# Kernel optimization log

Measured on AMD Instinct MI355X. Metric: run time of the kernel, lower is better.

## Reference

```python
import jax, jax.numpy as jnp
import numpy as np

B, H, W, C = 2, 128, 128, 96
L = H * W
NUM_HEADS = 6
D_STATE = 16
DT_RANK = 6  # ceil(96/16)
D_CONV = 4
MLP_HIDDEN = 4 * C


def _layernorm(x, g, b, eps=1e-5):
    m = x.mean(-1, keepdims=True)
    v = x.var(-1, keepdims=True)
    return (x - m) * jax.lax.rsqrt(v + eps) * g + b


def _dwconv2d(x, w, b):
    # x: [B,C,H,W], w: [C,1,3,3] depthwise, padding=1 (torch 'same' for k=3)
    y = jax.lax.conv_general_dilated(x, w, (1, 1), [(1, 1), (1, 1)],
                                     dimension_numbers=('NCHW', 'OIHW', 'NCHW'),
                                     feature_group_count=x.shape[1])
    return y + b[None, :, None, None]


def _dwconv1d(x, w):
    # x: [B,C,L], w: [C,1,4]; torch padding='same' for even k=4 pads (1,2); bias is None (conv_bias//2 == 0)
    return jax.lax.conv_general_dilated(x, w, (1,), [(1, 2)],
                                        dimension_numbers=('NCH', 'OIH', 'NCH'),
                                        feature_group_count=x.shape[1])


def _rope(x):
    # x: [b, H, W, c]; 2D axial rotary embedding, k_max = c//4 per axis
    b, h, w, c = x.shape
    k_max = c // 4
    theta = 1.0 / (10000.0 ** (jnp.arange(k_max, dtype=jnp.float32) / k_max))
    ang_h = jnp.broadcast_to(jnp.arange(h, dtype=jnp.float32)[:, None, None] * theta, (h, w, k_max))
    ang_w = jnp.broadcast_to(jnp.arange(w, dtype=jnp.float32)[None, :, None] * theta, (h, w, k_max))
    angles = jnp.concatenate([ang_h, ang_w], -1)  # [h,w,c//2]
    cos, sin = jnp.cos(angles), jnp.sin(angles)
    xr, xi = x[..., 0::2], x[..., 1::2]  # consecutive pairs -> complex
    out_r = xr * cos - xi * sin
    out_i = xr * sin + xi * cos
    return jnp.stack([out_r, out_i], -1).reshape(x.shape)


def _linear_attention(x, qk_w, qk_b, lepe_w, lepe_b):
    # x: [b, n, c]
    b, n, c = x.shape
    hd = c // NUM_HEADS
    qk = x @ qk_w + qk_b  # [b,n,2c]
    q = jax.nn.elu(qk[..., :c]) + 1.0
    k = jax.nn.elu(qk[..., c:]) + 1.0
    v = x
    q_r = _rope(q.reshape(b, H, W, c)).reshape(b, n, NUM_HEADS, hd).transpose(0, 2, 1, 3)
    k_r = _rope(k.reshape(b, H, W, c)).reshape(b, n, NUM_HEADS, hd).transpose(0, 2, 1, 3)
    qh = q.reshape(b, n, NUM_HEADS, hd).transpose(0, 2, 1, 3)
    kh = k.reshape(b, n, NUM_HEADS, hd).transpose(0, 2, 1, 3)
    vh = v.reshape(b, n, NUM_HEADS, hd).transpose(0, 2, 1, 3)
    kmean = kh.mean(axis=2, keepdims=True)  # [b,h,1,hd]
    zden = 1.0 / (jnp.einsum('bhnd,bhmd->bhnm', qh, kmean) + 1e-6)  # [b,h,n,1]
    scale = n ** (-0.5)
    kv = jnp.einsum('bhnd,bhne->bhde', k_r * scale, vh * scale)  # [b,h,hd,hd]
    out = jnp.einsum('bhnd,bhde->bhne', q_r, kv) * zden
    out = out.transpose(0, 2, 1, 3).reshape(b, n, c)
    v2d = v.reshape(b, H, W, c).transpose(0, 3, 1, 2)
    lepe = _dwconv2d(v2d, lepe_w, lepe_b).transpose(0, 2, 3, 1).reshape(b, n, c)
    return out + lepe


def _selective_scan(u, delta, A, Bm, Cm, Dv):
    # u, delta: [b,d,l]; A: [d,n]; Bm, Cm: [b,n,l]; Dv: [d]
    dA = jnp.exp(jnp.einsum('bdl,dn->lbdn', delta, A))
    dBu = jnp.einsum('bdl,bnl,bdl->lbdn', delta, Bm, u)
    Ct = jnp.moveaxis(Cm, -1, 0)  # [l,b,n]

    def step(hcar, inp):
        dA_t, dBu_t, C_t = inp
        hcar = dA_t * hcar + dBu_t  # [b,d,n]
        y_t = jnp.einsum('bdn,bn->bd', hcar, C_t)
        return hcar, y_t

    h0 = jnp.zeros(dA.shape[1:], dtype=u.dtype)
    _, ys = jax.lax.scan(step, h0, (dA, dBu, Ct))  # ys: [l,b,d]
    y = jnp.moveaxis(ys, 0, -1)  # [b,d,l]
    return y + Dv[None, :, None] * u


def setup_inputs() -> dict:
    key = jax.random.key(0)
    ks = iter(jax.random.split(key, 40))

    def rn(shape, s=0.02):
        return jax.random.normal(next(ks), shape, jnp.float32) * s

    dt = jnp.exp(jax.random.uniform(next(ks), (C,), jnp.float32)
                 * (np.log(0.1) - np.log(0.001)) + np.log(0.001))
    dt_proj_b = dt + jnp.log(-jnp.expm1(-dt))
    return {
        'hidden_states': jax.random.normal(next(ks), (B, L, C), jnp.float32),
        'norm_in_g': jnp.ones((C,), jnp.float32),
        'norm_in_b': jnp.zeros((C,), jnp.float32),
        'in_proj_w': rn((C, 3 * C)),
        'dw_w': rn((C, 1, 3, 3)),
        'dw_b': rn((C,)),
        'qk_w': rn((C, 2 * C)),
        'qk_b': rn((2 * C,)),
        'lepe_w': rn((C, 1, 3, 3)),
        'lepe_b': rn((C,)),
        'conv_x_w': rn((C, 1, D_CONV)),
        'conv_z_w': rn((C, 1, D_CONV)),
        'x_proj_w': rn((C, DT_RANK + 2 * D_STATE)),
        'dt_proj_w': rn((DT_RANK, C), DT_RANK ** -0.5),
        'dt_proj_b': dt_proj_b,
        'A_log': jnp.log(jnp.broadcast_to(jnp.arange(1, D_STATE + 1, dtype=jnp.float32), (C, D_STATE)) + 0.0),
        'D': jnp.ones((C,), jnp.float32),
        'out_proj_w': rn((2 * C, C)),
        'proj_out_w': rn((C, C)),
        'proj_out_b': rn((C,)),
        'out_w': rn((2 * C, C)),
        'out_b': rn((C,)),
        'norm_mlp_g': jnp.ones((C,), jnp.float32),
        'norm_mlp_b': jnp.zeros((C,), jnp.float32),
        'fc1_w': rn((C, MLP_HIDDEN)),
        'fc1_b': rn((MLP_HIDDEN,)),
        'fc2_w': rn((MLP_HIDDEN, C)),
        'fc2_b': rn((C,)),
    }


def reference(hidden_states, norm_in_g, norm_in_b, in_proj_w, dw_w, dw_b, qk_w, qk_b,
              lepe_w, lepe_b, conv_x_w, conv_z_w, x_proj_w, dt_proj_w, dt_proj_b,
              A_log, D, out_proj_w, proj_out_w, proj_out_b, out_w, out_b,
              norm_mlp_g, norm_mlp_b, fc1_w, fc1_b, fc2_w, fc2_b):
    b, l, c = hidden_states.shape
    shortcut = hidden_states
    hs = _layernorm(hidden_states, norm_in_g, norm_in_b)
    xzw = jnp.transpose(hs @ in_proj_w, (0, 2, 1))  # [b,3c,l]
    x, z, w_ = jnp.split(xzw, 3, axis=1)  # each [b,c,l]
    # linear-attention branch
    lin_x = jax.nn.silu(_dwconv2d(w_.reshape(b, c, H, W), dw_w, dw_b))
    lin_x = jnp.transpose(lin_x, (0, 2, 3, 1)).reshape(b, l, c)
    lin_x = _linear_attention(lin_x, qk_w, qk_b, lepe_w, lepe_b)
    # selective-scan branch
    A = -jnp.exp(A_log)
    x = jax.nn.silu(_dwconv1d(x, conv_x_w))
    z = jax.nn.silu(_dwconv1d(z, conv_z_w))
    x_dbl = jnp.einsum('bdl,de->ble', x, x_proj_w)
    dt = x_dbl[..., :DT_RANK]
    Bm = jnp.transpose(x_dbl[..., DT_RANK:DT_RANK + D_STATE], (0, 2, 1))
    Cm = jnp.transpose(x_dbl[..., DT_RANK + D_STATE:], (0, 2, 1))
    delta = jax.nn.softplus(jnp.einsum('blr,rd->bdl', dt, dt_proj_w) + dt_proj_b[None, :, None])
    y = _selective_scan(x, delta, A, Bm, Cm, D)
    y = jnp.concatenate([y, z], axis=1)  # [b,2c,l]
    out1 = jnp.transpose(y, (0, 2, 1)) @ out_proj_w  # [b,l,c]
    z_t = jnp.transpose(z, (0, 2, 1))
    out2 = (lin_x * z_t) @ proj_out_w + proj_out_b
    out = jnp.concatenate([out1, out2], -1) @ out_w + out_b
    out = shortcut + out
    h2 = _layernorm(out, norm_mlp_g, norm_mlp_b)
    h2 = jax.nn.gelu(h2 @ fc1_w + fc1_b, approximate=False)
    return out + (h2 @ fc2_w + fc2_b)
```

## Files before the change

kernel.cpp:

```cpp
#include <hip/hip_runtime.h>
#include <hip/hip_bf16.h>
#include <hip/hip_fp16.h>
#include <math.h>

#define B_ 2
#define H_ 128
#define W_ 128
#define C_ 96
#define L_ (H_*W_)
#define BL_ (B_*L_)
#define NH_ 6
#define NPROJ_ 38
#define MLPH_ 384
#define NCH_ 512
#define CHL_ (L_/NCH_)
#define NG_ 32

typedef __attribute__((ext_vector_type(8))) short bf16x8;
typedef __attribute__((ext_vector_type(4))) float f32x4;
typedef __attribute__((ext_vector_type(4))) unsigned short us4v;

#define MFMA16(a,b,c) __builtin_amdgcn_mfma_f32_16x16x32_bf16(a,b,c,0,0,0)

#define WOFF1 0
#define WOFF2 54
#define WOFF3 90
#define WOFF4 126
#define WOFF5 144
#define WOFF6 180
#define WOFF7 252
#define WOFF8 324
#define WFRAGS 333

__device__ __forceinline__ float siluf(float x){ return x / (1.f + __expf(-x)); }
__device__ __forceinline__ unsigned short f2bf(float x){
    __hip_bfloat16 h = __float2bfloat16(x);
    return *reinterpret_cast<unsigned short*>(&h);
}
__device__ __forceinline__ unsigned pack2(float a, float b){
    return (unsigned)f2bf(a) | ((unsigned)f2bf(b) << 16);
}
__device__ __forceinline__ float bf2f(unsigned short u){
    return __uint_as_float((unsigned)u << 16);
}
__device__ __forceinline__ unsigned short f2h(float x){
    __half h = __float2half(x);
    return *reinterpret_cast<unsigned short*>(&h);
}
__device__ __forceinline__ float h2f(unsigned short u){
    __half h = *reinterpret_cast<__half*>(&u);
    return __half2float(h);
}
__device__ __forceinline__ float gelu_fast(float x){
    float u_ = 0.7978845608f*x*(1.f + 0.044715f*x*x);
    float au = fabsf(u_);
    float e = __expf(-2.f*au);
    float th = (1.f - e)/(1.f + e);
    th = copysignf(th, u_);
    return 0.5f*x*(1.f + th);
}

__global__ __launch_bounds__(64) void k_setup(const float* __restrict__ w1,
    const float* __restrict__ w2, const float* __restrict__ w3,
    const float* __restrict__ w4, const float* __restrict__ w5,
    const float* __restrict__ w6, const float* __restrict__ w7,
    const float* __restrict__ dww, const float* __restrict__ lw,
    const float* __restrict__ xpw, const float* __restrict__ cxw,
    const float* __restrict__ czw,
    unsigned short* __restrict__ dst, float2* __restrict__ ctab,
    float* __restrict__ wt9, float* __restrict__ lw9, float* __restrict__ kvacc,
    float* __restrict__ wxT, float* __restrict__ wzT)
{
    int m = blockIdx.y;
    int l = threadIdx.x;
    if (m < 7){
        const float* srcs[7] = {w1,w2,w3,w4,w5,w6,w7};
        const int Ks[7]   = {96,96,192,96,192,96,384};
        const int Ns[7]   = {288,192,96,96,96,384,96};
        const int offs[7] = {WOFF1,WOFF2,WOFF3,WOFF4,WOFF5,WOFF6,WOFF7};
        int f = blockIdx.x;
        int nnt = Ns[m] >> 4, nkf = Ks[m] >> 5;
        if (f >= nnt*nkf) return;
        int kf = f / nnt, nt = f - kf*nnt;
        const float* s = srcs[m];
        unsigned short* d = dst + ((size_t)(offs[m] + f)*64 + l)*8;
        int krow = kf*32 + (l>>4)*8;
        int col  = nt*16 + (l&15);
        #pragma unroll
        for (int j=0;j<8;j++) d[j] = f2bf(s[(size_t)(krow+j)*Ns[m] + col]);
    } else {
        int x = blockIdx.x;
        if (x == 0){
            for (int i=l; i<128*24; i+=64){
                int pos = i/24, p = i%24;
                float th = powf(10000.f, -(float)p/24.f);
                float sn, cs; sincosf((float)pos*th, &sn, &cs);
                ctab[i] = make_float2(cs, sn);
            }
        } else if (x == 1){
            for (int i=l; i<3264; i+=64) kvacc[i] = 0.f;
        } else if (x == 2){
            for (int i=l; i<864; i+=64){
                int c = i/9, tap = i%9;
                wt9[tap*96 + c] = dww[i];
                lw9[tap*96 + c] = lw[i];
            }
        } else if (x == 3){
            for (int f=0; f<9; f++){
                int kf=f/3, nt=f%3;
                unsigned short* d = dst + ((size_t)(WOFF8 + f)*64 + l)*8;
                int krow = kf*32 + (l>>4)*8;
                int col  = nt*16 + (l&15);
                #pragma unroll
                for (int j=0;j<8;j++){
                    float v = (col < NPROJ_) ? xpw[(size_t)(krow+j)*NPROJ_ + col] : 0.f;
                    d[j] = f2bf(v);
                }
            }
        } else if (x == 4){
            for (int i=l; i<384; i+=64){
                int j = i/96, c = i%96;
                wxT[i] = cxw[c*4 + j];
                wzT[i] = czw[c*4 + j];
            }
        }
    }
}

__global__ __launch_bounds__(256) void k_ln_inproj_m(const float* __restrict__ hs,
    const float* __restrict__ gg, const float* __restrict__ bb,
    const unsigned short* __restrict__ wbf,
    unsigned short* __restrict__ xx, unsigned short* __restrict__ zz,
    unsigned short* __restrict__ ww)
{
    __shared__ unsigned short A[64*128];
    int t = threadIdx.x;
    size_t row0 = (size_t)blockIdx.x * 64;
    {
        int r = t >> 2, q = t & 3;
        const float* src = hs + (row0 + r)*C_ + q*24;
        float v[24];
        float s=0.f, s2=0.f;
        #pragma unroll
        for (int i=0;i<24;i++){ float x=src[i]; v[i]=x; s+=x; s2+=x*x; }
        s += __shfl_xor(s,1); s2 += __shfl_xor(s2,1);
        s += __shfl_xor(s,2); s2 += __shfl_xor(s2,2);
        float mn = s*(1.f/C_);
        float rs = rsqrtf(s2*(1.f/C_) - mn*mn + 1e-5f);
        int base = r*128, sw = (r&7)<<3;
        #pragma unroll
        for (int i=0;i<24;i+=2){
            int c = q*24 + i;
            float a0 = (v[i]  -mn)*rs*gg[c]   + bb[c];
            float a1 = (v[i+1]-mn)*rs*gg[c+1] + bb[c+1];
            *(unsigned*)&A[base + (c ^ sw)] = pack2(a0,a1);
        }
    }
    __syncthreads();
    int w = t>>6, l = t&63, lr = l&15, lh = l>>4;
    int arow = w*16 + lr;
    int abase = arow*128, asw = (arow&7)<<3;
    bf16x8 af[3];
    #pragma unroll
    for (int kf=0;kf<3;kf++)
        af[kf] = *(const bf16x8*)&A[abase + ((kf*32 + lh*8) ^ asw)];
    #pragma unroll 2
    for (int nt=0; nt<18; nt++){
        f32x4 acc = {0.f,0.f,0.f,0.f};
        #pragma unroll
        for (int kf=0;kf<3;kf++){
            bf16x8 bf_ = *(const bf16x8*)(wbf + ((size_t)((WOFF1 + kf*18 + nt)*64 + l))*8);
            acc = MFMA16(af[kf], bf_, acc);
        }
        unsigned short* base_;
        if (nt < 6) base_ = xx; else if (nt < 12) base_ = zz; else base_ = ww;
        int col = (nt%6)*16 + lr;
        unsigned short* dst = base_ + (row0 + w*16 + lh*4)*C_ + col;
        #pragma unroll
        for (int j=0;j<4;j++) dst[(size_t)j*C_] = f2bf(acc[j]);
    }
}

__global__ __launch_bounds__(256) void k_dwconv2d(const unsigned short* __restrict__ wwb,
    const float* __restrict__ wt9, const float* __restrict__ dwb,
    unsigned short* __restrict__ out)
{
    int gid = blockIdx.x*256 + threadIdx.x;
    int row = gid/24, c4 = gid%24; int c = c4*4;
    int b = row >> 14;
    int ll = row & (L_-1);
    int h = ll >> 7, wq = ll & 127;
    float a0=0.f,a1=0.f,a2=0.f,a3=0.f;
    #pragma unroll
    for (int kh=0; kh<3; kh++){
        int hh = h + kh - 1;
        if ((unsigned)hh < 128u){
            int base_row = (b<<14) + (hh<<7);
            #pragma unroll
            for (int kw=0; kw<3; kw++){
                int wp = wq + kw - 1;
                if ((unsigned)wp < 128u){
                    us4v v = *(const us4v*)&wwb[(size_t)(base_row + wp)*C_ + c];
                    float4 wt = *(const float4*)&wt9[(kh*3+kw)*96 + c];
                    a0 += bf2f(v[0])*wt.x; a1 += bf2f(v[1])*wt.y;
                    a2 += bf2f(v[2])*wt.z; a3 += bf2f(v[3])*wt.w;
                }
            }
        }
    }
    float4 bv = *(const float4*)&dwb[c];
    us4v o;
    o[0]=f2bf(siluf(a0+bv.x)); o[1]=f2bf(siluf(a1+bv.y));
    o[2]=f2bf(siluf(a2+bv.z)); o[3]=f2bf(siluf(a3+bv.w));
    *(us4v*)&out[(size_t)row*C_ + c] = o;
}

__global__ __launch_bounds__(384) void k_conv1d_xdbl(const unsigned short* __restrict__ xxb,
    const unsigned short* __restrict__ zzb, const float* __restrict__ wxT,
    const float* __restrict__ wzT, const unsigned short* __restrict__ wbf,
    const float* __restrict__ dtw, const float* __restrict__ dtb,
    const float* __restrict__ A_log,
    unsigned short* __restrict__ xsb, unsigned short* __restrict__ zb,
    unsigned short* __restrict__ dlh, float* __restrict__ BC,
    float* __restrict__ Ap, float* __restrict__ Be)
{
    __shared__ unsigned short A[64*128];
    __shared__ float XD[64][8];
    __shared__ float dtws[6][96];
    __shared__ float sdl[64][96];
    __shared__ float sbc[64][32];
    int t = threadIdx.x;
    size_t row0 = (size_t)blockIdx.x * 64;
    int b = (int)(row0 >> 14);
    int l0 = (int)(row0 & 16383);
    for (int i=t; i<576; i+=384) dtws[i/96][i%96] = dtw[i];
    for (int p=t; p<64*24; p+=384){
        int r = p/24, cq = p - r*24, c = cq*4;
        int l = l0 + r;
        float ax0=0.f,ax1=0.f,ax2=0.f,ax3=0.f;
        float az0=0.f,az1=0.f,az2=0.f,az3=0.f;
        #pragma unroll
        for (int j=0;j<4;j++){
            int lq = l - 1 + j;
            if ((unsigned)lq < (unsigned)L_){
                size_t off = ((size_t)(b<<14) + lq)*C_ + c;
                us4v xv = *(const us4v*)&xxb[off];
                us4v zv = *(const us4v*)&zzb[off];
// ... 47 lines not shown
        int r = t>>2, q = t&3;
        float xd0=XD[r][0], xd1=XD[r][1], xd2=XD[r][2];
        float xd3=XD[r][3], xd4=XD[r][4], xd5=XD[r][5];
        #pragma unroll
        for (int g=0; g<6; g++){
            int c = q*24 + g*4;
            float4 acc = *(const float4*)&dtb[c];
            float4 w0 = *(const float4*)&dtws[0][c];
            float4 w1 = *(const float4*)&dtws[1][c];
            float4 w2 = *(const float4*)&dtws[2][c];
            float4 w3 = *(const float4*)&dtws[3][c];
            float4 w4 = *(const float4*)&dtws[4][c];
            float4 w5 = *(const float4*)&dtws[5][c];
            acc.x += xd0*w0.x + xd1*w1.x + xd2*w2.x + xd3*w3.x + xd4*w4.x + xd5*w5.x;
            acc.y += xd0*w0.y + xd1*w1.y + xd2*w2.y + xd3*w3.y + xd4*w4.y + xd5*w5.y;
            acc.z += xd0*w0.z + xd1*w1.z + xd2*w2.z + xd3*w3.z + xd4*w4.z + xd5*w5.z;
            acc.w += xd0*w0.w + xd1*w1.w + xd2*w2.w + xd3*w3.w + xd4*w4.w + xd5*w5.w;
            float4 dl;
            dl.x = (acc.x>20.f)? acc.x : __logf(1.f+__expf(acc.x));
            dl.y = (acc.y>20.f)? acc.y : __logf(1.f+__expf(acc.y));
            dl.z = (acc.z>20.f)? acc.z : __logf(1.f+__expf(acc.z));
            dl.w = (acc.w>20.f)? acc.w : __logf(1.f+__expf(acc.w));
            sdl[r][c]=dl.x; sdl[r][c+1]=dl.y; sdl[r][c+2]=dl.z; sdl[r][c+3]=dl.w;
            us4v dh; dh[0]=f2h(dl.x); dh[1]=f2h(dl.y); dh[2]=f2h(dl.z); dh[3]=f2h(dl.w);
            *(us4v*)&dlh[(row0+r)*C_ + c] = dh;
        }
    }
    __syncthreads();
    {
        int c = t>>2, nq = t&3;
        float4 a4 = *(const float4*)&A_log[c*16 + nq*4];
        float a0=-__expf(a4.x), a1=-__expf(a4.y), a2=-__expf(a4.z), a3=-__expf(a4.w);
        int chbase = b*NCH_ + (l0>>5);
        int csw_c = c;
        #pragma unroll
        for (int chunk=0; chunk<2; chunk++){
            float ap0=1.f,ap1=1.f,ap2=1.f,ap3=1.f;
            float be0=0.f,be1=0.f,be2=0.f,be3=0.f;
            for (int i=0;i<CHL_;i++){
                int row = chunk*CHL_ + i;
                float dl = sdl[row][c];
                float u = bf2f(A[row*128 + (csw_c ^ ((row&7)<<3))]);
                float du = dl*u;
                float4 bc = *(const float4*)&sbc[row][nq*4];
                float e0=__expf(dl*a0), e1=__expf(dl*a1), e2=__expf(dl*a2), e3=__expf(dl*a3);
                ap0*=e0; be0=be0*e0+du*bc.x;
                ap1*=e1; be1=be1*e1+du*bc.y;
                ap2*=e2; be2=be2*e2+du*bc.z;
                ap3*=e3; be3=be3*e3+du*bc.w;
            }
            size_t o = (size_t)(chbase+chunk)*1536 + c*16 + nq*4;
            float4 apv={ap0,ap1,ap2,ap3}, bev={be0,be1,be2,be3};
            *(float4*)&Ap[o] = apv;
            *(float4*)&Be[o] = bev;
        }
    }
}

__global__ __launch_bounds__(256) void k_qk_kv(const unsigned short* __restrict__ lin,
    const unsigned short* __restrict__ wbf, const float* __restrict__ qkb,
    const float2* __restrict__ ctab, unsigned short* __restrict__ qo,
    float* __restrict__ kvacc)
{
    __shared__ unsigned short A[64*128];
    __shared__ float KR[64*105];
    __shared__ float kmsum[96];
    int t = threadIdx.x;
    size_t row0 = (size_t)blockIdx.x * 64;
    int b = (int)(row0 >> 14);
    int l0 = (int)(row0 & 16383);
    for (int p = t; p < 64*12; p += 256){
        int r = p/12, c = (p - r*12)*8;
        int sw = (r&7)<<3;
        *(uint4*)&A[r*128 + (c ^ sw)] = *(const uint4*)&lin[(row0+r)*C_ + c];
    }
    if (t < 96) kmsum[t] = 0.f;
    __syncthreads();
    int w=t>>6, l=t&63, lr=l&15, lh=l>>4;
    int arow = w*16+lr; int asw=(arow&7)<<3;
    bf16x8 af[3];
    #pragma unroll
    for (int kf=0;kf<3;kf++)
        af[kf] = *(const bf16x8*)&A[arow*128 + ((kf*32 + lh*8) ^ asw)];
    #pragma unroll 2
    for (int nt=0; nt<12; nt++){
        f32x4 acc={0.f,0.f,0.f,0.f};
        #pragma unroll
        for (int kf=0;kf<3;kf++){
            bf16x8 bfr=*(const bf16x8*)(wbf + ((size_t)((WOFF2 + kf*12 + nt)*64 + l))*8);
            acc = MFMA16(af[kf], bfr, acc);
        }
        int colg = nt*16 + lr;
        float bias = qkb[colg];
        float vv[4];
        #pragma unroll
        for (int j=0;j<4;j++){
            float v = acc[j] + bias;
            vv[j] = (v>0.f)? v+1.f : __expf(v);
        }
        if (nt < 6){
            unsigned short* dp = qo + (row0 + w*16 + lh*4)*C_ + colg;
            #pragma unroll
            for (int j=0;j<4;j++) dp[(size_t)j*C_] = f2bf(vv[j]);
        } else {
            int ck = colg - 96;
            atomicAdd(&kmsum[ck], vv[0]+vv[1]+vv[2]+vv[3]);
            float pv[4];
// ... 104 lines not shown
                    acc.z += bf2f(v[2])*wt.z; acc.w += bf2f(v[3])*wt.w;
                }
            }
        }
    }
    us4v zu = *(const us4v*)&zb[row*C_ + c];
    us4v res;
    res[0] = f2bf((o.x*zd + acc.x)*bf2f(zu[0]));
    res[1] = f2bf((o.y*zd + acc.y)*bf2f(zu[1]));
    res[2] = f2bf((o.z*zd + acc.z)*bf2f(zu[2]));
    res[3] = f2bf((o.w*zd + acc.w)*bf2f(zu[3]));
    *(us4v*)&azb[row*C_ + c] = res;
}

__global__ __launch_bounds__(384) void k_scan2a(const float* __restrict__ Ap,
    const float* __restrict__ Be, float* __restrict__ GA, float* __restrict__ GB)
{
    int t = threadIdx.x; int blk = blockIdx.x;
    int b = blk>>5, g = blk&(NG_-1);
    int idx = (t>>2)*16 + (t&3)*4;
    float4 A = {1.f,1.f,1.f,1.f}, Bv = {0.f,0.f,0.f,0.f};
    for (int j=0;j<16;j++){
        size_t o = ((size_t)(b*NCH_ + g*16 + j))*1536 + idx;
        float4 a = *(const float4*)&Ap[o];
        float4 bb = *(const float4*)&Be[o];
        Bv.x=a.x*Bv.x+bb.x; Bv.y=a.y*Bv.y+bb.y; Bv.z=a.z*Bv.z+bb.z; Bv.w=a.w*Bv.w+bb.w;
        A.x*=a.x; A.y*=a.y; A.z*=a.z; A.w*=a.w;
    }
    size_t o = (size_t)blk*1536 + idx;
    *(float4*)&GA[o] = A;
    *(float4*)&GB[o] = Bv;
}

__global__ __launch_bounds__(256) void k_scan2b(const float* __restrict__ GA,
    const float* __restrict__ GB, float* __restrict__ Gin)
{
    int t = blockIdx.x*256 + threadIdx.x;
    int b = t/1536, m = t%1536;
    float h = 0.f;
    for (int g=0; g<NG_; g++){
        size_t o = ((size_t)(b*NG_+g))*1536 + m;
        Gin[o] = h;
        h = GA[o]*h + GB[o];
    }
}

__global__ __launch_bounds__(384) void k_scan2c(const float* __restrict__ Ap,
    const float* __restrict__ Be, const float* __restrict__ Gin,
    float* __restrict__ Hin)
{
    int t = threadIdx.x; int blk = blockIdx.x;
    int b = blk>>5, g = blk&(NG_-1);
    int idx = (t>>2)*16 + (t&3)*4;
    float4 h = *(const float4*)&Gin[(size_t)blk*1536 + idx];
    for (int j=0;j<16;j++){
        size_t o = ((size_t)(b*NCH_ + g*16 + j))*1536 + idx;
        *(float4*)&Hin[o] = h;
        float4 a = *(const float4*)&Ap[o];
        float4 bb = *(const float4*)&Be[o];
        h.x=a.x*h.x+bb.x; h.y=a.y*h.y+bb.y; h.z=a.z*h.z+bb.z; h.w=a.w*h.w+bb.w;
    }
}

__global__ __launch_bounds__(384) void k_scan3(const unsigned short* __restrict__ dlh,
    const unsigned short* __restrict__ xsb, const float* __restrict__ BC,
    const float* __restrict__ A_log, const float* __restrict__ Dv,
    const float* __restrict__ Hin, unsigned short* __restrict__ y)
{
    int t = threadIdx.x; int nq = t&3, c = t>>2;
    int blk = blockIdx.x; int b = blk>>9, ch = blk&(NCH_-1);
    float4 a4 = *(const float4*)&A_log[c*16 + nq*4];
    float a0=-__expf(a4.x), a1=-__expf(a4.y), a2=-__expf(a4.z), a3=-__expf(a4.w);
    float4 h = *(const float4*)&Hin[(size_t)blk*1536 + c*16 + nq*4];
    float Dc = Dv[c];
    size_t base = ((size_t)b<<14) + ch*CHL_;
    for (int i=0;i<CHL_;i++){
        size_t row = base + i;
        float dl = h2f(dlh[row*C_+c]);
        float u  = bf2f(xsb[row*C_+c]);
        float du = dl*u;
        float4 bcB = *(const float4*)&BC[row*32 + nq*4];
        float4 bcC = *(const float4*)&BC[row*32 + 16 + nq*4];
        float e0=__expf(dl*a0), e1=__expf(dl*a1), e2=__expf(dl*a2), e3=__expf(dl*a3);
        h.x=h.x*e0+du*bcB.x; h.y=h.y*e1+du*bcB.y;
        h.z=h.z*e2+du*bcB.z; h.w=h.w*e3+du*bcB.w;
        float yv = h.x*bcC.x + h.y*bcC.y + h.z*bcC.z + h.w*bcC.w;
        yv += __shfl_xor(yv,1);
        yv += __shfl_xor(yv,2);
        if (nq == 0) y[row*C_+c] = f2bf(yv + Dc*u);
    }
}

__global__ __launch_bounds__(512) void k_combine_mlp(const unsigned short* __restrict__ yb,
    const unsigned short* __restrict__ zb, const unsigned short* __restrict__ azb,
    const unsigned short* __restrict__ wbf, const float* __restrict__ pob,
    const float* __restrict__ outb, const float* __restrict__ hs,
    const float* __restrict__ gg, const float* __restrict__ bb,
    const float* __restrict__ f1b, const float* __restrict__ f2b,
    float* __restrict__ outr)
{
    __shared__ __attribute__((aligned(16))) char POOL[65536];
    __shared__ float LNS[64][2], LNS2[64][2];
    unsigned short* C2 = (unsigned short*)POOL;
    unsigned short* AT = (unsigned short*)POOL;
    unsigned short* HID= (unsigned short*)(POOL + 16384);
    int t=threadIdx.x;
    size_t row0=(size_t)blockIdx.x*64;
    int w=t>>6, l=t&63, lr=l&15, lh=l>>4;
    int rt=w>>1, hf=w&1;
    int arow=rt*16+lr; int asw=(arow&7)<<3;
    size_t gbase = (row0+arow)*C_;
    bf16x8 af1[6], af2[3];
    #pragma unroll
    for (int kf=0;kf<3;kf++){
        af1[kf]   = *(const bf16x8*)&yb[gbase + kf*32 + lh*8];
        af1[3+kf] = *(const bf16x8*)&zb[gbase + kf*32 + lh*8];
        af2[kf]   = *(const bf16x8*)&azb[gbase + kf*32 + lh*8];
    }
    #pragma unroll
    for (int q=0;q<3;q++){
        int nt = hf*3 + q;
        f32x4 a1={0.f,0.f,0.f,0.f}, a2={0.f,0.f,0.f,0.f};
        #pragma unroll
        for (int kf=0;kf<6;kf++){
            bf16x8 b=*(const bf16x8*)(wbf+((size_t)((WOFF3+kf*6+nt)*64+l))*8);
            a1=MFMA16(af1[kf],b,a1);
        }
        #pragma unroll
        for (int kf=0;kf<3;kf++){
            bf16x8 b=*(const bf16x8*)(wbf+((size_t)((WOFF4+kf*6+nt)*64+l))*8);
            a2=MFMA16(af2[kf],b,a2);
        }
        int col=nt*16+lr;
        float pb=pob[col];
        #pragma unroll
        for (int j=0;j<4;j++){
            int row=rt*16+lh*4+j;
            int sw2=(row&7)<<3;
            C2[row*192 + (col^sw2)] = f2bf(a1[j]);
            C2[row*192 + ((96+col)^sw2)] = f2bf(a2[j]+pb);
        }
    }
    __syncthreads();
    bf16x8 af3[6];
    #pragma unroll
    for (int kf=0;kf<6;kf++) af3[kf]=*(const bf16x8*)&C2[arow*192 + ((kf*32+lh*8)^asw)];
    float outv[3][4];
    #pragma unroll
    for (int q=0;q<3;q++){
        int nt = hf*3 + q;
        f32x4 acc={0.f,0.f,0.f,0.f};
        #pragma unroll
        for (int kf=0;kf<6;kf++){
            bf16x8 b=*(const bf16x8*)(wbf+((size_t)((WOFF5+kf*6+nt)*64+l))*8);
            acc=MFMA16(af3[kf],b,acc);
        }
        int col=nt*16+lr;
        float ob=outb[col];
        #pragma unroll
        for (int j=0;j<4;j++){
            size_t row=row0+rt*16+lh*4+j;
            outv[q][j] = acc[j] + ob + hs[row*C_+col];
        }
    }
    float s_[4], s2_[4];
    #pragma unroll
    for (int j=0;j<4;j++){
        float s=0.f, s2=0.f;
        #pragma unroll
        for (int q=0;q<3;q++){ float v=outv[q][j]; s+=v; s2+=v*v; }
        s_[j]=s; s2_[j]=s2;
    }
    #pragma unroll
    for (int m=1;m<16;m<<=1){
        #pragma unroll
        for (int j=0;j<4;j++){
            s_[j]  += __shfl_xor(s_[j],  m);
            s2_[j] += __shfl_xor(s2_[j], m);
        }
    }
    if (lr==0){
        #pragma unroll
        for (int j=0;j<4;j++){
            int row = rt*16+lh*4+j;
            LNS[row][hf]  = s_[j];
            LNS2[row][hf] = s2_[j];
        }
    }
    __syncthreads();
    #pragma unroll
    for (int j=0;j<4;j++){
        int row = rt*16+lh*4+j;
        float s  = LNS[row][0]  + LNS[row][1];
        float s2 = LNS2[row][0] + LNS2[row][1];
        float mn = s*(1.f/C_);
        float rs = rsqrtf(s2*(1.f/C_) - mn*mn + 1e-5f);
        int sw2 = (row&7)<<3;
        #pragma unroll
        for (int q=0;q<3;q++){
            int col = (hf*3+q)*16+lr;
            AT[row*128 + (col^sw2)] = f2bf((outv[q][j]-mn)*rs*gg[col]+bb[col]);
        }
    }
    __syncthreads();
    {
        bf16x8 af[3];
        #pragma unroll
        for(int kf=0;kf<3;kf++) af[kf]=*(const bf16x8*)&AT[arow*128+((kf*32+lh*8)^asw)];
        #pragma unroll 2
        for(int q=0;q<12;q++){
            int nt = hf*12 + q;
            f32x4 acc={0.f,0.f,0.f,0.f};
            #pragma unroll
            for(int kf=0;kf<3;kf++){
                bf16x8 b=*(const bf16x8*)(wbf+((size_t)((WOFF6+kf*24+nt)*64+l))*8);
                acc=MFMA16(af[kf],b,acc);
            }
            int col=nt*16+lr;
            float bias=f1b[col];
            #pragma unroll
            for(int j=0;j<4;j++){
                int row=rt*16+lh*4+j;
                HID[row*384 + (col^((row&7)<<3))] = f2bf(gelu_fast(acc[j]+bias));
            }
        }
    }
    __syncthreads();
    {
        bf16x8 afh[12];
        #pragma unroll
        for(int kf=0;kf<12;kf++) afh[kf]=*(const bf16x8*)&HID[arow*384+((kf*32+lh*8)^asw)];
        #pragma unroll
        for(int q=0;q<3;q++){
            int nt = hf*3 + q;
            f32x4 acc={0.f,0.f,0.f,0.f};
            #pragma unroll
            for(int kf=0;kf<12;kf++){
                bf16x8 b=*(const bf16x8*)(wbf+((size_t)((WOFF7+kf*6+nt)*64+l))*8);
                acc=MFMA16(afh[kf],b,acc);
            }
            int col=nt*16+lr;
            float bias=f2b[col];
            #pragma unroll
            for(int j=0;j<4;j++){
                size_t row=row0+rt*16+lh*4+j;
                outr[row*C_+col] = outv[q][j] + acc[j] + bias;
            }
        }
    }
}

extern "C" void kernel_launch(void* const* d_in, const int* in_sizes, int n_in,
                              void* d_out, int out_size, void* d_ws, size_t ws_size,
                              hipStream_t stream)
{
    const float* hs        = (const float*)d_in[0];
    const float* norm_in_g = (const float*)d_in[1];
    const float* norm_in_b = (const float*)d_in[2];
    const float* in_proj_w = (const float*)d_in[3];
    const float* dw_w      = (const float*)d_in[4];
    const float* dw_b      = (const float*)d_in[5];
    const float* qk_w      = (const float*)d_in[6];
    const float* qk_b      = (const float*)d_in[7];
    const float* lepe_w    = (const float*)d_in[8];
    const float* lepe_b    = (const float*)d_in[9];
    const float* conv_x_w  = (const float*)d_in[10];
    const float* conv_z_w  = (const float*)d_in[11];
    const float* x_proj_w  = (const float*)d_in[12];
    const float* dt_proj_w = (const float*)d_in[13];
    const float* dt_proj_b = (const float*)d_in[14];
    const float* A_log     = (const float*)d_in[15];
    const float* Dv        = (const float*)d_in[16];
    const float* out_proj_w= (const float*)d_in[17];
    const float* proj_out_w= (const float*)d_in[18];
    const float* proj_out_b= (const float*)d_in[19];
    const float* out_w     = (const float*)d_in[20];
    const float* out_b     = (const float*)d_in[21];
    const float* norm_mlp_g= (const float*)d_in[22];
    const float* norm_mlp_b= (const float*)d_in[23];
    const float* fc1_w     = (const float*)d_in[24];
    const float* fc1_b     = (const float*)d_in[25];
    const float* fc2_w     = (const float*)d_in[26];
    const float* fc2_b     = (const float*)d_in[27];

    float* ws = (float*)d_ws;
    size_t o = 0;
    const size_t USH = (size_t)BL_*C_/2;
    unsigned short* xxb  = (unsigned short*)(ws + o); o += USH;
    unsigned short* zzb  = (unsigned short*)(ws + o); o += USH;
    unsigned short* wwb  = (unsigned short*)(ws + o); o += USH;
    unsigned short* linb = (unsigned short*)(ws + o); o += USH;
    unsigned short* zbuf = (unsigned short*)(ws + o); o += USH;
    unsigned short* xsb  = (unsigned short*)(ws + o); o += USH;
    unsigned short* dlh  = (unsigned short*)(ws + o); o += USH;
    float* BC    = ws + o; o += (size_t)BL_*32;
    float* Ap    = ws + o; o += (size_t)B_*NCH_*1536;
    float* Be    = ws + o; o += (size_t)B_*NCH_*1536;
    float* Hin   = ws + o; o += (size_t)B_*NCH_*1536;
    float* GA    = ws + o; o += (size_t)B_*NG_*1536;
    float* GB    = ws + o; o += (size_t)B_*NG_*1536;
    float* Gin   = ws + o; o += (size_t)B_*NG_*1536;
    float* kvacc = ws + o; o += 3264;
    float2* ctab = (float2*)(ws + o); o += 6144;
    float* wt9   = ws + o; o += 864;
    float* lw9   = ws + o; o += 864;
    float* wxT   = ws + o; o += 384;
    float* wzT   = ws + o; o += 384;
    unsigned short* wbf = (unsigned short*)(ws + o);

    unsigned short* qb  = xxb;
    unsigned short* yb  = zzb;
    unsigned short* azb = wwb;
    float* outr = (float*)d_out;

    k_setup<<<dim3(72,8), 64, 0, stream>>>(in_proj_w, qk_w, out_proj_w, proj_out_w,
                                           out_w, fc1_w, fc2_w, dw_w, lepe_w,
                                           x_proj_w, conv_x_w, conv_z_w,
                                           wbf, ctab, wt9, lw9, kvacc, wxT, wzT);
    k_ln_inproj_m<<<BL_/64, 256, 0, stream>>>(hs, norm_in_g, norm_in_b, wbf,
                                              xxb, zzb, wwb);
    k_dwconv2d<<<(BL_*24)/256, 256, 0, stream>>>(wwb, wt9, dw_b, linb);
    k_conv1d_xdbl<<<BL_/64, 384, 0, stream>>>(xxb, zzb, wxT, wzT, wbf,
                                              dt_proj_w, dt_proj_b, A_log,
                                              xsb, zbuf, dlh, BC, Ap, Be);
    k_qk_kv<<<BL_/64, 256, 0, stream>>>(linb, wbf, qk_b, ctab, qb, kvacc);
    k_attnout<<<BL_/16, 384, 0, stream>>>(qb, linb, zbuf, kvacc, ctab, lw9, lepe_b, azb);
    k_scan2a<<<B_*NG_, 384, 0, stream>>>(Ap, Be, GA, GB);
    k_scan2b<<<12, 256, 0, stream>>>(GA, GB, Gin);
    k_scan2c<<<B_*NG_, 384, 0, stream>>>(Ap, Be, Gin, Hin);
    k_scan3<<<B_*NCH_, 384, 0, stream>>>(dlh, xsb, BC, A_log, Dv, Hin, yb);
    k_combine_mlp<<<BL_/64, 512, 0, stream>>>(yb, zbuf, azb, wbf, proj_out_b,
                                              out_b, hs, norm_mlp_g, norm_mlp_b,
                                              fc1_b, fc2_b, outr);
}
```

Baseline: 185.5 us.

## Fuse dwconv2d into qk_kv, merge scan2b into scan2c, cache bf16 residual

The depthwise 3x3 conv and SiLU now run inside k_qk_kv's tile-load loop, so the separate launch and the reload of linb from global memory go away. linb is still written for the later attention-output kernel. The scan2b serial prefix over groups is merged into scan2c: each block recomputes its own group prefix from GA/GB, which removes a launch and the Gin buffer but adds redundant work. The residual input is stored as bf16 during the LayerNorm pass and read back in bf16 in the final combine, which halves that read but lowers the residual's precision.

Measured after the change: 192.2 us. 3.6% more time.

```diff
diff --git a/kernel.cpp b/kernel.cpp
--- a/kernel.cpp
+++ b/kernel.cpp
@@ -131,7 +131,7 @@
     const float* __restrict__ gg, const float* __restrict__ bb,
     const unsigned short* __restrict__ wbf,
     unsigned short* __restrict__ xx, unsigned short* __restrict__ zz,
-    unsigned short* __restrict__ ww)
+    unsigned short* __restrict__ ww, unsigned short* __restrict__ hsb)
 {
     __shared__ unsigned short A[64*128];
     int t = threadIdx.x;
@@ -143,6 +143,13 @@
         float s=0.f, s2=0.f;
         #pragma unroll
         for (int i=0;i<24;i++){ float x=src[i]; v[i]=x; s+=x; s2+=x*x; }
+        unsigned short* hdst = hsb + (row0 + r)*C_ + q*24;
+        #pragma unroll
+        for (int i=0;i<24;i+=4){
+            us4v hv; hv[0]=f2bf(v[i]); hv[1]=f2bf(v[i+1]);
+            hv[2]=f2bf(v[i+2]); hv[3]=f2bf(v[i+3]);
+            *(us4v*)&hdst[i] = hv;
+        }
         s += __shfl_xor(s,1); s2 += __shfl_xor(s2,1);
         s += __shfl_xor(s,2); s2 += __shfl_xor(s2,2);
         float mn = s*(1.f/C_);
@@ -179,40 +186,6 @@
         #pragma unroll
         for (int j=0;j<4;j++) dst[(size_t)j*C_] = f2bf(acc[j]);
     }
-}
-
-__global__ __launch_bounds__(256) void k_dwconv2d(const unsigned short* __restrict__ wwb,
-    const float* __restrict__ wt9, const float* __restrict__ dwb,
-    unsigned short* __restrict__ out)
-{
-    int gid = blockIdx.x*256 + threadIdx.x;
-    int row = gid/24, c4 = gid%24; int c = c4*4;
-    int b = row >> 14;
-    int ll = row & (L_-1);
-    int h = ll >> 7, wq = ll & 127;
-    float a0=0.f,a1=0.f,a2=0.f,a3=0.f;
-    #pragma unroll
-    for (int kh=0; kh<3; kh++){
-        int hh = h + kh - 1;
-        if ((unsigned)hh < 128u){
-            int base_row = (b<<14) + (hh<<7);
-            #pragma unroll
-            for (int kw=0; kw<3; kw++){
-                int wp = wq + kw - 1;
-                if ((unsigned)wp < 128u){
-                    us4v v = *(const us4v*)&wwb[(size_t)(base_row + wp)*C_ + c];
-                    float4 wt = *(const float4*)&wt9[(kh*3+kw)*96 + c];
-                    a0 += bf2f(v[0])*wt.x; a1 += bf2f(v[1])*wt.y;
-                    a2 += bf2f(v[2])*wt.z; a3 += bf2f(v[3])*wt.w;
-                }
-            }
-        }
-    }
-    float4 bv = *(const float4*)&dwb[c];
-    us4v o;
-    o[0]=f2bf(siluf(a0+bv.x)); o[1]=f2bf(siluf(a1+bv.y));
-    o[2]=f2bf(siluf(a2+bv.z)); o[3]=f2bf(siluf(a3+bv.w));
-    *(us4v*)&out[(size_t)row*C_ + c] = o;
 }
 
 __global__ __launch_bounds__(384) void k_conv1d_xdbl(const unsigned short* __restrict__ xxb,
@@ -351,10 +324,11 @@
     }
 }
 
-__global__ __launch_bounds__(256) void k_qk_kv(const unsigned short* __restrict__ lin,
+__global__ __launch_bounds__(256) void k_qk_kv(const unsigned short* __restrict__ wwb,
+    const float* __restrict__ wt9, const float* __restrict__ dwb,
     const unsigned short* __restrict__ wbf, const float* __restrict__ qkb,
-    const float2* __restrict__ ctab, unsigned short* __restrict__ qo,
-    float* __restrict__ kvacc)
+    const float2* __restrict__ ctab, unsigned short* __restrict__ linb,
+    unsigned short* __restrict__ qo, float* __restrict__ kvacc)
 {
     __shared__ unsigned short A[64*128];
     __shared__ float KR[64*105];
@@ -363,10 +337,35 @@
     size_t row0 = (size_t)blockIdx.x * 64;
     int b = (int)(row0 >> 14);
     int l0 = (int)(row0 & 16383);
-    for (int p = t; p < 64*12; p += 256){
-        int r = p/12, c = (p - r*12)*8;
+    for (int p = t; p < 64*24; p += 256){
+        int r = p/24, cq = p - r*24, c = cq*4;
+        int ll = l0 + r;
+        int hq = ll>>7, wq = ll&127;
+        float a0=0.f,a1=0.f,a2=0.f,a3=0.f;
+        #pragma unroll
+        for (int kh=0; kh<3; kh++){
+            int hh = hq + kh - 1;
+            if ((unsigned)hh < 128u){
+                int base_row = (b<<14) + (hh<<7);
+                #pragma unroll
+                for (int kw=0; kw<3; kw++){
+                    int wp = wq + kw - 1;
+                    if ((unsigned)wp < 128u){
+                        us4v v = *(const us4v*)&wwb[(size_t)(base_row + wp)*C_ + c];
+                        float4 wt = *(const float4*)&wt9[(kh*3+kw)*96 + c];
+                        a0 += bf2f(v[0])*wt.x; a1 += bf2f(v[1])*wt.y;
+                        a2 += bf2f(v[2])*wt.z; a3 += bf2f(v[3])*wt.w;
+                    }
+                }
+            }
+        }
+        float4 bv = *(const float4*)&dwb[c];
+        us4v o;
+        o[0]=f2bf(siluf(a0+bv.x)); o[1]=f2bf(siluf(a1+bv.y));
+        o[2]=f2bf(siluf(a2+bv.z)); o[3]=f2bf(siluf(a3+bv.w));
+        *(us4v*)&linb[(row0+r)*C_ + c] = o;
         int sw = (r&7)<<3;
-        *(uint4*)&A[r*128 + (c ^ sw)] = *(const uint4*)&lin[(row0+r)*C_ + c];
+        *(us4v*)&A[r*128 + (c ^ sw)] = o;
     }
     if (t < 96) kmsum[t] = 0.f;
     __syncthreads();
@@ -537,27 +536,20 @@
     *(float4*)&GB[o] = Bv;
 }
 
-__global__ __launch_bounds__(256) void k_scan2b(const float* __restrict__ GA,
-    const float* __restrict__ GB, float* __restrict__ Gin)
-{
-    int t = blockIdx.x*256 + threadIdx.x;
-    int b = t/1536, m = t%1536;
-    float h = 0.f;
-    for (int g=0; g<NG_; g++){
-        size_t o = ((size_t)(b*NG_+g))*1536 + m;
-        Gin[o] = h;
-        h = GA[o]*h + GB[o];
-    }
-}
-
-__global__ __launch_bounds__(384) void k_scan2c(const float* __restrict__ Ap,
-    const float* __restrict__ Be, const float* __restrict__ Gin,
-    float* __restrict__ Hin)
+__global__ __launch_bounds__(384) void k_scan2bc(const float* __restrict__ Ap,
+    const float* __restrict__ Be, const float* __restrict__ GA,
+    const float* __restrict__ GB, float* __restrict__ Hin)
 {
     int t = threadIdx.x; int blk = blockIdx.x;
     int b = blk>>5, g = blk&(NG_-1);
     int idx = (t>>2)*16 + (t&3)*4;
-    float4 h = *(const float4*)&Gin[(size_t)blk*1536 + idx];
+    float4 h = {0.f,0.f,0.f,0.f};
+    for (int gg=0; gg<g; gg++){
+        size_t o = ((size_t)(b*NG_+gg))*1536 + idx;
+        float4 a = *(const float4*)&GA[o];
+        float4 bb = *(const float4*)&GB[o];
+        h.x=a.x*h.x+bb.x; h.y=a.y*h.y+bb.y; h.z=a.z*h.z+bb.z; h.w=a.w*h.w+bb.w;
+    }
     for (int j=0;j<16;j++){
         size_t o = ((size_t)(b*NCH_ + g*16 + j))*1536 + idx;
         *(float4*)&Hin[o] = h;
@@ -599,7 +591,7 @@
 __global__ __launch_bounds__(512) void k_combine_mlp(const unsigned short* __restrict__ yb,
     const unsigned short* __restrict__ zb, const unsigned short* __restrict__ azb,
     const unsigned short* __restrict__ wbf, const float* __restrict__ pob,
-    const float* __restrict__ outb, const float* __restrict__ hs,
+    const float* __restrict__ outb, const unsigned short* __restrict__ hsb,
     const float* __restrict__ gg, const float* __restrict__ bb,
     const float* __restrict__ f1b, const float* __restrict__ f2b,
     float* __restrict__ outr)
@@ -665,7 +657,7 @@
         #pragma unroll
         for (int j=0;j<4;j++){
             size_t row=row0+rt*16+lh*4+j;
-            outv[q][j] = acc[j] + ob + hs[row*C_+col];
+            outv[q][j] = acc[j] + ob + bf2f(hsb[row*C_+col]);
         }
     }
     float s_[4], s2_[4];
@@ -798,13 +790,13 @@
     unsigned short* zbuf = (unsigned short*)(ws + o); o += USH;
     unsigned short* xsb  = (unsigned short*)(ws + o); o += USH;
     unsigned short* dlh  = (unsigned short*)(ws + o); o += USH;
+    unsigned short* hsb  = (unsigned short*)(ws + o); o += USH;
     float* BC    = ws + o; o += (size_t)BL_*32;
     float* Ap    = ws + o; o += (size_t)B_*NCH_*1536;
     float* Be    = ws + o; o += (size_t)B_*NCH_*1536;
     float* Hin   = ws + o; o += (size_t)B_*NCH_*1536;
     float* GA    = ws + o; o += (size_t)B_*NG_*1536;
     float* GB    = ws + o; o += (size_t)B_*NG_*1536;
-    float* Gin   = ws + o; o += (size_t)B_*NG_*1536;
     float* kvacc = ws + o; o += 3264;
     float2* ctab = (float2*)(ws + o); o += 6144;
     float* wt9   = ws + o; o += 864;
@@ -823,18 +815,17 @@
                                            x_proj_w, conv_x_w, conv_z_w,
                                            wbf, ctab, wt9, lw9, kvacc, wxT, wzT);
     k_ln_inproj_m<<<BL_/64, 256, 0, stream>>>(hs, norm_in_g, norm_in_b, wbf,
-                                              xxb, zzb, wwb);
-    k_dwconv2d<<<(BL_*24)/256, 256, 0, stream>>>(wwb, wt9, dw_b, linb);
+                                              xxb, zzb, wwb, hsb);
     k_conv1d_xdbl<<<BL_/64, 384, 0, stream>>>(xxb, zzb, wxT, wzT, wbf,
                                               dt_proj_w, dt_proj_b, A_log,
                                               xsb, zbuf, dlh, BC, Ap, Be);
-    k_qk_kv<<<BL_/64, 256, 0, stream>>>(linb, wbf, qk_b, ctab, qb, kvacc);
+    k_qk_kv<<<BL_/64, 256, 0, stream>>>(wwb, wt9, dw_b, wbf, qk_b, ctab,
+                                        linb, qb, kvacc);
     k_attnout<<<BL_/16, 384, 0, stream>>>(qb, linb, zbuf, kvacc, ctab, lw9, lepe_b, azb);
     k_scan2a<<<B_*NG_, 384, 0, stream>>>(Ap, Be, GA, GB);
-    k_scan2b<<<12, 256, 0, stream>>>(GA, GB, Gin);
-    k_scan2c<<<B_*NG_, 384, 0, stream>>>(Ap, Be, Gin, Hin);
+    k_scan2bc<<<B_*NG_, 384, 0, stream>>>(Ap, Be, GA, GB, Hin);
     k_scan3<<<B_*NCH_, 384, 0, stream>>>(dlh, xsb, BC, A_log, Dv, Hin, yb);
     k_combine_mlp<<<BL_/64, 512, 0, stream>>>(yb, zbuf, azb, wbf, proj_out_b,
-                                              out_b, hs, norm_mlp_g, norm_mlp_b,
+                                              out_b, hsb, norm_mlp_g, norm_mlp_b,
                                               fc1_b, fc2_b, outr);
 }
```

## Split MLP hidden layer into two halves to shrink shared memory in combine kernel

Applied to the files above, without the earlier changes.

The fused combine+MLP kernel now computes the 384-wide hidden activation in two 192-column halves. Each half's fc2 contribution accumulates in registers. This cuts the shared-memory pool from 64KB to 40KB and halves the register array for hidden fragments, aiming for higher occupancy. In exchange it adds extra block-wide barriers per half and keeps fc2 accumulators live across both halves. A trivial variable alias in the scan kernel is also removed.

Result: no change. 187.5 us (+1.1%).

```diff
diff --git a/kernel.cpp b/kernel.cpp
--- a/kernel.cpp
+++ b/kernel.cpp
@@ -326,7 +326,6 @@
         float4 a4 = *(const float4*)&A_log[c*16 + nq*4];
         float a0=-__expf(a4.x), a1=-__expf(a4.y), a2=-__expf(a4.z), a3=-__expf(a4.w);
         int chbase = b*NCH_ + (l0>>5);
-        int csw_c = c;
         #pragma unroll
         for (int chunk=0; chunk<2; chunk++){
             float ap0=1.f,ap1=1.f,ap2=1.f,ap3=1.f;
@@ -334,7 +333,7 @@
             for (int i=0;i<CHL_;i++){
                 int row = chunk*CHL_ + i;
                 float dl = sdl[row][c];
-                float u = bf2f(A[row*128 + (csw_c ^ ((row&7)<<3))]);
+                float u = bf2f(A[row*128 + (c ^ ((row&7)<<3))]);
                 float du = dl*u;
                 float4 bc = *(const float4*)&sbc[row][nq*4];
                 float e0=__expf(dl*a0), e1=__expf(dl*a1), e2=__expf(dl*a2), e3=__expf(dl*a3);
@@ -604,7 +603,7 @@
     const float* __restrict__ f1b, const float* __restrict__ f2b,
     float* __restrict__ outr)
 {
-    __shared__ __attribute__((aligned(16))) char POOL[65536];
+    __shared__ __attribute__((aligned(16))) char POOL[40960];
     __shared__ float LNS[64][2], LNS2[64][2];
     unsigned short* C2 = (unsigned short*)POOL;
     unsigned short* AT = (unsigned short*)POOL;
@@ -708,49 +707,56 @@
         }
     }
     __syncthreads();
-    {
-        bf16x8 af[3];
-        #pragma unroll
-        for(int kf=0;kf<3;kf++) af[kf]=*(const bf16x8*)&AT[arow*128+((kf*32+lh*8)^asw)];
+    bf16x8 afa[3];
+    #pragma unroll
+    for(int kf=0;kf<3;kf++) afa[kf]=*(const bf16x8*)&AT[arow*128+((kf*32+lh*8)^asw)];
+    f32x4 acc2[3];
+    #pragma unroll
+    for (int q=0;q<3;q++) acc2[q] = (f32x4){0.f,0.f,0.f,0.f};
+    #pragma unroll
+    for (int half=0; half<2; half++){
         #pragma unroll 2
-        for(int q=0;q<12;q++){
-            int nt = hf*12 + q;
+        for(int q=0;q<6;q++){
+            int ntg = half*12 + hf*6 + q;
             f32x4 acc={0.f,0.f,0.f,0.f};
             #pragma unroll
             for(int kf=0;kf<3;kf++){
-                bf16x8 b=*(const bf16x8*)(wbf+((size_t)((WOFF6+kf*24+nt)*64+l))*8);
-                acc=MFMA16(af[kf],b,acc);
-            }
-            int col=nt*16+lr;
-            float bias=f1b[col];
+                bf16x8 b=*(const bf16x8*)(wbf+((size_t)((WOFF6+kf*24+ntg)*64+l))*8);
+                acc=MFMA16(afa[kf],b,acc);
+            }
+            int colg=ntg*16+lr;
+            int coll=colg - half*192;
+            float bias=f1b[colg];
             #pragma unroll
             for(int j=0;j<4;j++){
                 int row=rt*16+lh*4+j;
-                HID[row*384 + (col^((row&7)<<3))] = f2bf(gelu_fast(acc[j]+bias));
-            }
-        }
-    }
-    __syncthreads();
-    {
-        bf16x8 afh[12];
-        #pragma unroll
-        for(int kf=0;kf<12;kf++) afh[kf]=*(const bf16x8*)&HID[arow*384+((kf*32+lh*8)^asw)];
+                HID[row*192 + (coll^((row&7)<<3))] = f2bf(gelu_fast(acc[j]+bias));
+            }
+        }
+        __syncthreads();
+        bf16x8 afh[6];
+        #pragma unroll
+        for(int kf=0;kf<6;kf++) afh[kf]=*(const bf16x8*)&HID[arow*192+((kf*32+lh*8)^asw)];
         #pragma unroll
         for(int q=0;q<3;q++){
             int nt = hf*3 + q;
-            f32x4 acc={0.f,0.f,0.f,0.f};
-            #pragma unroll
-            for(int kf=0;kf<12;kf++){
-                bf16x8 b=*(const bf16x8*)(wbf+((size_t)((WOFF7+kf*6+nt)*64+l))*8);
-                acc=MFMA16(afh[kf],b,acc);
-            }
-            int col=nt*16+lr;
-            float bias=f2b[col];
-            #pragma unroll
-            for(int j=0;j<4;j++){
-                size_t row=row0+rt*16+lh*4+j;
-                outr[row*C_+col] = outv[q][j] + acc[j] + bias;
-            }
+            #pragma unroll
+            for(int kf=0;kf<6;kf++){
+                bf16x8 b=*(const bf16x8*)(wbf+((size_t)((WOFF7+(half*6+kf)*6+nt)*64+l))*8);
+                acc2[q]=MFMA16(afh[kf],b,acc2[q]);
+            }
+        }
+        __syncthreads();
+    }
+    #pragma unroll
+    for(int q=0;q<3;q++){
+        int nt = hf*3 + q;
+        int col=nt*16+lr;
+        float bias=f2b[col];
+        #pragma unroll
+        for(int j=0;j<4;j++){
+            size_t row=row0+rt*16+lh*4+j;
+            outr[row*C_+col] = outv[q][j] + acc2[q][j] + bias;
         }
     }
 }
```

## Fold out_proj and proj_out into out_w via precomputed combined weights

Applied to the files above, without the earlier changes.

The setup kernel now multiplies out_proj_w·out_w[:96] and proj_out_w·out_w[96:] into combined bf16 MFMA weight fragments and folds proj_out_b into a combined bias. The combine kernel drops the intermediate GEMM, its shared-memory staging and a block barrier, and accumulates both branch inputs straight into the final output projection. This removes one chained matmul stage per tile. In exchange the setup kernel does small serial fp32 dot products at every call, and rounding changes because the intermediate bf16 rounding of C2 no longer happens.

Result: no change. 183.4 us (median of 2 runs) (-1.1%).

```diff
diff --git a/kernel.cpp b/kernel.cpp
--- a/kernel.cpp
+++ b/kernel.cpp
@@ -24,13 +24,12 @@
 
 #define WOFF1 0
 #define WOFF2 54
-#define WOFF3 90
-#define WOFF4 126
-#define WOFF5 144
-#define WOFF6 180
-#define WOFF7 252
-#define WOFF8 324
-#define WFRAGS 333
+#define WOFF6 90
+#define WOFF7 162
+#define WOFF8 234
+#define WOFF9 243
+#define WOFFA 279
+#define WFRAGS 297
 
 __device__ __forceinline__ float siluf(float x){ return x / (1.f + __expf(-x)); }
 __device__ __forceinline__ unsigned short f2bf(float x){
@@ -61,24 +60,26 @@
 }
 
 __global__ __launch_bounds__(64) void k_setup(const float* __restrict__ w1,
-    const float* __restrict__ w2, const float* __restrict__ w3,
-    const float* __restrict__ w4, const float* __restrict__ w5,
-    const float* __restrict__ w6, const float* __restrict__ w7,
+    const float* __restrict__ w2, const float* __restrict__ w6,
+    const float* __restrict__ w7,
     const float* __restrict__ dww, const float* __restrict__ lw,
     const float* __restrict__ xpw, const float* __restrict__ cxw,
     const float* __restrict__ czw,
+    const float* __restrict__ opw, const float* __restrict__ poww,
+    const float* __restrict__ outw, const float* __restrict__ pob,
+    const float* __restrict__ outb,
     unsigned short* __restrict__ dst, float2* __restrict__ ctab,
     float* __restrict__ wt9, float* __restrict__ lw9, float* __restrict__ kvacc,
-    float* __restrict__ wxT, float* __restrict__ wzT)
+    float* __restrict__ wxT, float* __restrict__ wzT, float* __restrict__ bias2)
 {
     int m = blockIdx.y;
     int l = threadIdx.x;
-    if (m < 7){
-        const float* srcs[7] = {w1,w2,w3,w4,w5,w6,w7};
-        const int Ks[7]   = {96,96,192,96,192,96,384};
-        const int Ns[7]   = {288,192,96,96,96,384,96};
-        const int offs[7] = {WOFF1,WOFF2,WOFF3,WOFF4,WOFF5,WOFF6,WOFF7};
-        int f = blockIdx.x;
+    int f = blockIdx.x;
+    if (m < 4){
+        const float* srcs[4] = {w1,w2,w6,w7};
+        const int Ks[4]   = {96,96,96,384};
+        const int Ns[4]   = {288,192,384,96};
+        const int offs[4] = {WOFF1,WOFF2,WOFF6,WOFF7};
         int nnt = Ns[m] >> 4, nkf = Ks[m] >> 5;
         if (f >= nnt*nkf) return;
         int kf = f / nnt, nt = f - kf*nnt;
@@ -88,8 +89,8 @@
         int col  = nt*16 + (l&15);
         #pragma unroll
         for (int j=0;j<8;j++) d[j] = f2bf(s[(size_t)(krow+j)*Ns[m] + col]);
-    } else {
-        int x = blockIdx.x;
+    } else if (m == 4){
+        int x = f;
         if (x == 0){
             for (int i=l; i<128*24; i+=64){
                 int pos = i/24, p = i%24;
@@ -106,9 +107,9 @@
                 lw9[tap*96 + c] = lw[i];
             }
         } else if (x == 3){
-            for (int f=0; f<9; f++){
-                int kf=f/3, nt=f%3;
-                unsigned short* d = dst + ((size_t)(WOFF8 + f)*64 + l)*8;
+            for (int ff=0; ff<9; ff++){
+                int kf=ff/3, nt=ff%3;
+                unsigned short* d = dst + ((size_t)(WOFF8 + ff)*64 + l)*8;
                 int krow = kf*32 + (l>>4)*8;
                 int col  = nt*16 + (l&15);
                 #pragma unroll
@@ -123,6 +124,38 @@
                 wxT[i] = cxw[c*4 + j];
                 wzT[i] = czw[c*4 + j];
             }
+        } else if (x == 5){
+            for (int c=l; c<96; c+=64){
+                float acc = outb[c];
+                for (int k=0;k<96;k++) acc += pob[k]*outw[(size_t)(96+k)*96 + c];
+                bias2[c] = acc;
+            }
+        }
+    } else if (m == 5){
+        if (f >= 36) return;
+        int kf = f/6, nt = f%6;
+        unsigned short* d = dst + ((size_t)(WOFF9 + f)*64 + l)*8;
+        int krow = kf*32 + (l>>4)*8;
+        int col  = nt*16 + (l&15);
+        #pragma unroll
+        for (int j=0;j<8;j++){
+            float acc = 0.f;
+            const float* oprow = &opw[(size_t)(krow+j)*96];
+            for (int k=0;k<96;k++) acc += oprow[k]*outw[(size_t)k*96 + col];
+            d[j] = f2bf(acc);
+        }
+    } else {
+        if (f >= 18) return;
+        int kf = f/6, nt = f%6;
+        unsigned short* d = dst + ((size_t)(WOFFA + f)*64 + l)*8;
+        int krow = kf*32 + (l>>4)*8;
+        int col  = nt*16 + (l&15);
+        #pragma unroll
+        for (int j=0;j<8;j++){
+            float acc = 0.f;
+            const float* porow = &poww[(size_t)(krow+j)*96];
+            for (int k=0;k<96;k++) acc += porow[k]*outw[(size_t)(96+k)*96 + col];
+            d[j] = f2bf(acc);
         }
     }
 }
@@ -326,7 +359,6 @@
         float4 a4 = *(const float4*)&A_log[c*16 + nq*4];
         float a0=-__expf(a4.x), a1=-__expf(a4.y), a2=-__expf(a4.z), a3=-__expf(a4.w);
         int chbase = b*NCH_ + (l0>>5);
-        int csw_c = c;
         #pragma unroll
         for (int chunk=0; chunk<2; chunk++){
             float ap0=1.f,ap1=1.f,ap2=1.f,ap3=1.f;
@@ -334,7 +366,7 @@
             for (int i=0;i<CHL_;i++){
                 int row = chunk*CHL_ + i;
                 float dl = sdl[row][c];
-                float u = bf2f(A[row*128 + (csw_c ^ ((row&7)<<3))]);
+                float u = bf2f(A[row*128 + (c ^ ((row&7)<<3))]);
                 float du = dl*u;
                 float4 bc = *(const float4*)&sbc[row][nq*4];
                 float e0=__expf(dl*a0), e1=__expf(dl*a1), e2=__expf(dl*a2), e3=__expf(dl*a3);
@@ -598,15 +630,13 @@
 
 __global__ __launch_bounds__(512) void k_combine_mlp(const unsigned short* __restrict__ yb,
     const unsigned short* __restrict__ zb, const unsigned short* __restrict__ azb,
-    const unsigned short* __restrict__ wbf, const float* __restrict__ pob,
-    const float* __restrict__ outb, const float* __restrict__ hs,
-    const float* __restrict__ gg, const float* __restrict__ bb,
-    const float* __restrict__ f1b, const float* __restrict__ f2b,
-    float* __restrict__ outr)
+    const unsigned short* __restrict__ wbf, const float* __restrict__ bias2,
+    const float* __restrict__ hs, const float* __restrict__ gg,
+    const float* __restrict__ bb, const float* __restrict__ f1b,
+    const float* __restrict__ f2b, float* __restrict__ outr)
 {
     __shared__ __attribute__((aligned(16))) char POOL[65536];
     __shared__ float LNS[64][2], LNS2[64][2];
-    unsigned short* C2 = (unsigned short*)POOL;
     unsigned short* AT = (unsigned short*)POOL;
     unsigned short* HID= (unsigned short*)(POOL + 16384);
     int t=threadIdx.x;
@@ -622,34 +652,6 @@
         af1[3+kf] = *(const bf16x8*)&zb[gbase + kf*32 + lh*8];
         af2[kf]   = *(const bf16x8*)&azb[gbase + kf*32 + lh*8];
     }
-    #pragma unroll
-    for (int q=0;q<3;q++){
-        int nt = hf*3 + q;
-        f32x4 a1={0.f,0.f,0.f,0.f}, a2={0.f,0.f,0.f,0.f};
-        #pragma unroll
-        for (int kf=0;kf<6;kf++){
-            bf16x8 b=*(const bf16x8*)(wbf+((size_t)((WOFF3+kf*6+nt)*64+l))*8);
-            a1=MFMA16(af1[kf],b,a1);
-        }
-        #pragma unroll
-        for (int kf=0;kf<3;kf++){
-            bf16x8 b=*(const bf16x8*)(wbf+((size_t)((WOFF4+kf*6+nt)*64+l))*8);
-            a2=MFMA16(af2[kf],b,a2);
-        }
-        int col=nt*16+lr;
-        float pb=pob[col];
-        #pragma unroll
-        for (int j=0;j<4;j++){
-            int row=rt*16+lh*4+j;
-            int sw2=(row&7)<<3;
-            C2[row*192 + (col^sw2)] = f2bf(a1[j]);
-            C2[row*192 + ((96+col)^sw2)] = f2bf(a2[j]+pb);
-        }
-    }
-    __syncthreads();
-    bf16x8 af3[6];
-    #pragma unroll
-    for (int kf=0;kf<6;kf++) af3[kf]=*(const bf16x8*)&C2[arow*192 + ((kf*32+lh*8)^asw)];
     float outv[3][4];
     #pragma unroll
     for (int q=0;q<3;q++){
@@ -657,15 +659,20 @@
         f32x4 acc={0.f,0.f,0.f,0.f};
         #pragma unroll
         for (int kf=0;kf<6;kf++){
-            bf16x8 b=*(const bf16x8*)(wbf+((size_t)((WOFF5+kf*6+nt)*64+l))*8);
-            acc=MFMA16(af3[kf],b,acc);
+            bf16x8 b=*(const bf16x8*)(wbf+((size_t)((WOFF9+kf*6+nt)*64+l))*8);
+            acc=MFMA16(af1[kf],b,acc);
+        }
+        #pragma unroll
+        for (int kf=0;kf<3;kf++){
+            bf16x8 b=*(const bf16x8*)(wbf+((size_t)((WOFFA+kf*6+nt)*64+l))*8);
+            acc=MFMA16(af2[kf],b,acc);
         }
         int col=nt*16+lr;
-        float ob=outb[col];
+        float b2v=bias2[col];
         #pragma unroll
         for (int j=0;j<4;j++){
             size_t row=row0+rt*16+lh*4+j;
-            outv[q][j] = acc[j] + ob + hs[row*C_+col];
+            outv[q][j] = acc[j] + b2v + hs[row*C_+col];
         }
     }
     float s_[4], s2_[4];
@@ -811,6 +818,7 @@
     float* lw9   = ws + o; o += 864;
     float* wxT   = ws + o; o += 384;
     float* wzT   = ws + o; o += 384;
+    float* bias2 = ws + o; o += 96;
     unsigned short* wbf = (unsigned short*)(ws + o);
 
     unsigned short* qb  = xxb;
@@ -818,10 +826,11 @@
     unsigned short* azb = wwb;
     float* outr = (float*)d_out;
 
-    k_setup<<<dim3(72,8), 64, 0, stream>>>(in_proj_w, qk_w, out_proj_w, proj_out_w,
-                                           out_w, fc1_w, fc2_w, dw_w, lepe_w,
-                                           x_proj_w, conv_x_w, conv_z_w,
-                                           wbf, ctab, wt9, lw9, kvacc, wxT, wzT);
+    k_setup<<<dim3(72,7), 64, 0, stream>>>(in_proj_w, qk_w, fc1_w, fc2_w,
+                                           dw_w, lepe_w, x_proj_w, conv_x_w, conv_z_w,
+                                           out_proj_w, proj_out_w, out_w,
+                                           proj_out_b, out_b,
+                                           wbf, ctab, wt9, lw9, kvacc, wxT, wzT, bias2);
     k_ln_inproj_m<<<BL_/64, 256, 0, stream>>>(hs, norm_in_g, norm_in_b, wbf,
                                               xxb, zzb, wwb);
     k_dwconv2d<<<(BL_*24)/256, 256, 0, stream>>>(wwb, wt9, dw_b, linb);
@@ -834,7 +843,7 @@
     k_scan2b<<<12, 256, 0, stream>>>(GA, GB, Gin);
     k_scan2c<<<B_*NG_, 384, 0, stream>>>(Ap, Be, Gin, Hin);
     k_scan3<<<B_*NCH_, 384, 0, stream>>>(dlh, xsb, BC, A_log, Dv, Hin, yb);
-    k_combine_mlp<<<BL_/64, 512, 0, stream>>>(yb, zbuf, azb, wbf, proj_out_b,
-                                              out_b, hs, norm_mlp_g, norm_mlp_b,
+    k_combine_mlp<<<BL_/64, 512, 0, stream>>>(yb, zbuf, azb, wbf, bias2,
+                                              hs, norm_mlp_g, norm_mlp_b,
                                               fc1_b, fc2_b, outr);
 }
```
